# Optimization experiments

Hardware: AMD Instinct MI355X
Metric: run time of the kernel (lower is better)

## Reference

```python
import jax, jax.numpy as jnp
import numpy as np

B, T, D = 1, 4096, 1024
H, DK, DV, L = 16, 64, 64, 32
ROT_SCALE = 1.0  # rotary_pos_scale default


def _rotate_half(x):
    # '... (j d) -> ... j d' with j=2, then cat((-x2, x1))
    x1, x2 = jnp.split(x, 2, axis=-1)
    return jnp.concatenate((-x2, x1), axis=-1)


def _apply_rope(freqs, x, scale):
    # freqs: [T, L] broadcasts over leading dims of x [..., T, L]
    return x * jnp.cos(freqs) * scale + _rotate_half(x) * jnp.sin(freqs) * scale


def setup_inputs() -> dict:
    key = jax.random.key(0)
    ks = jax.random.split(key, 9)
    q = jax.random.normal(ks[0], (B, T, D), jnp.float32)
    k = jax.random.normal(ks[1], (B, T, D), jnp.float32)
    v = jax.random.normal(ks[2], (B, T, D), jnp.float32)
    mask = jnp.tril(jnp.ones((T, T), dtype=bool))  # causal [T, T]
    rotary_freqs = jax.random.normal(ks[3], (T, L), jnp.float32)
    s = 0.02
    w_q = jax.random.normal(ks[4], (H * DK, D), jnp.float32) * s
    w_k = jax.random.normal(ks[5], (H * DK, D), jnp.float32) * s
    w_v = jax.random.normal(ks[6], (H * DV, D), jnp.float32) * s
    w_o = jax.random.normal(ks[7], (D, H * DV), jnp.float32) * s
    return {"q": q, "k": k, "v": v, "mask": mask, "rotary_freqs": rotary_freqs,
            "w_q": w_q, "w_k": w_k, "w_v": w_v, "w_o": w_o}


def reference(q, k, v, mask, rotary_freqs, w_q, w_k, w_v, w_o):
    # project and split heads: '... T (H k) -> ... H T k'
    def heads(x, w, dh):
        y = jnp.einsum('btd,ed->bte', x, w)
        return y.reshape(B, T, H, dh).transpose(0, 2, 1, 3)  # [B,H,T,dh]

    q_i = heads(q, w_q, DK)
    k_i = heads(k, w_k, DK)
    v_i = heads(v, w_v, DV)

    # rotary pos emb on first L dims of q, k AND v (unusual: v too)
    q_scale, k_scale = ROT_SCALE, ROT_SCALE ** (-1.0)

    def rope(x, scale):
        xl, xr = x[..., :L], x[..., L:]
        return jnp.concatenate((_apply_rope(rotary_freqs, xl, scale), xr), axis=-1)

    q_i = rope(q_i, q_scale)
    k_i = rope(k_i, k_scale)
    v_i = rope(v_i, k_scale)

    s_qk = jnp.einsum('bhik,bhjk->bhij', q_i, k_i) / (DK ** 0.5)
    neg = -jnp.finfo(s_qk.dtype).max
    s_qk = jnp.where(mask, s_qk, neg)  # mask broadcasts [T,T] -> [B,H,T,T]
    attn = jax.nn.softmax(s_qk, axis=-1)
    vals = jnp.einsum('bhij,bhjv->bhiv', attn, v_i)
    vals = vals.transpose(0, 2, 1, 3).reshape(B, T, H * DV)  # '... H T v -> ... T (H v)'
    out = jnp.einsum('bte,oe->bto', vals, w_o)
    return out
```

## Files before the change

kernel.cpp:

```cpp
#include <hip/hip_runtime.h>

typedef unsigned short u16;
typedef unsigned int u32;
typedef short bf16x8 __attribute__((ext_vector_type(8)));
typedef float f32x4 __attribute__((ext_vector_type(4)));
typedef unsigned short u16x4 __attribute__((ext_vector_type(4)));
typedef unsigned short u16x8 __attribute__((ext_vector_type(8)));

__device__ __forceinline__ u16 f32_to_bf16(float f) {
    u32 u = __float_as_uint(f);
    u += 0x7FFFu + ((u >> 16) & 1u);
    return (u16)(u >> 16);
}
__device__ __forceinline__ short f32_to_bf16_trunc(float f) {
    return (short)(__float_as_uint(f) >> 16);
}

__device__ __forceinline__ void gl_lds16(const u16* g, u16* l) {
    __builtin_amdgcn_global_load_lds(
        (const __attribute__((address_space(1))) u32*)g,
        (__attribute__((address_space(3))) u32*)l, 16, 0, 0);
}

struct CastArgs {
    const float* src[7];
    u16* dst[7];
    int n4[7];
};

__global__ __launch_bounds__(256) void cast_kernel(CastArgs a) {
    const int y = blockIdx.y;
    const float* s = a.src[y];
    u16* d = a.dst[y];
    const int n4 = a.n4[y];
    for (int i = blockIdx.x * blockDim.x + threadIdx.x; i < n4; i += gridDim.x * blockDim.x) {
        f32x4 v = *(const f32x4*)&s[(size_t)i * 4];
        u16x4 o = { f32_to_bf16(v[0]), f32_to_bf16(v[1]), f32_to_bf16(v[2]), f32_to_bf16(v[3]) };
        *(u16x4*)&d[(size_t)i * 4] = o;
    }
}

#define GK 1024
#define GN 1024
#define GM 4096

__global__ __launch_bounds__(256) void gemm_rope(
    const u16* __restrict__ A0, const u16* __restrict__ A1, const u16* __restrict__ A2,
    const u16* __restrict__ W0, const u16* __restrict__ W1, const u16* __restrict__ W2,
    u16* __restrict__ C0, u16* __restrict__ C1, u16* __restrict__ C2,
    const float* __restrict__ freqs)
{
    __shared__ u16 SM[8192];
    u16* As = SM;
    u16* Bs = SM + 4096;

    const int z = blockIdx.z;
    const u16* A = (z == 0) ? A0 : ((z == 1) ? A1 : A2);
    const u16* W = (z == 0) ? W0 : ((z == 1) ? W1 : W2);
    u16* Cb      = (z == 0) ? C0 : ((z == 1) ? C1 : C2);
    const float ascale = (z == 0) ? 0.125f : 1.0f;

    const int tid  = threadIdx.x;
    const int w    = tid >> 6;
    const int lane = tid & 63;
    const int quad = lane >> 4;
    const int l16  = lane & 15;
    const int m0 = blockIdx.x * 128;
    const int n0 = blockIdx.y * 128;
    const int wm = (w >> 1) * 64;
    const int wn = (w & 1) * 64;

    const int sr = tid >> 2;
    const int sc = (tid & 3) * 8;
    const size_t aoff0 = (size_t)(m0 + sr) * GK + sc;
    const size_t aoff1 = aoff0 + (size_t)64 * GK;
    const size_t boff0 = (size_t)(n0 + sr) * GK + sc;
    const size_t boff1 = boff0 + (size_t)64 * GK;
    u16* ldsA0 = &As[w * 512];
    u16* ldsA1 = &As[2048 + w * 512];
    u16* ldsB0 = &Bs[w * 512];
    u16* ldsB1 = &Bs[2048 + w * 512];

    f32x4 acc[4][4];
    for (int i = 0; i < 4; i++)
        for (int j = 0; j < 4; j++) acc[i][j] = 0.f;

    for (int k0 = 0; k0 < GK; k0 += 32) {
        gl_lds16(A + aoff0 + k0, ldsA0);
        gl_lds16(A + aoff1 + k0, ldsA1);
        gl_lds16(W + boff0 + k0, ldsB0);
        gl_lds16(W + boff1 + k0, ldsB1);
        __syncthreads();

        bf16x8 af[4], bfr[4];
        for (int t = 0; t < 4; t++) {
            af[t]  = *(const bf16x8*)&As[(wm + t * 16 + l16) * 32 + quad * 8];
            bfr[t] = *(const bf16x8*)&Bs[(wn + t * 16 + l16) * 32 + quad * 8];
        }
        for (int mt = 0; mt < 4; mt++)
            for (int nt = 0; nt < 4; nt++)
                acc[mt][nt] = __builtin_amdgcn_mfma_f32_16x16x32_bf16(
                    af[mt], bfr[nt], acc[mt][nt], 0, 0, 0);
        __syncthreads();
    }
    u16* tr = SM + w * 1152;

    const int hh = (n0 + wn) >> 6;
    const size_t tb = (size_t)hh * 262144 + (size_t)((m0 + wm) >> 6) * 4096;

    if (z != 2) {
        for (int mt = 0; mt < 4; mt++) {
            #pragma unroll
            for (int r = 0; r < 4; r++) {
                int m = m0 + wm + mt * 16 + quad * 4 + r;
                float v0 = acc[mt][0][r];
                float v1 = acc[mt][1][r];
                float f0 = freqs[m * 32 + l16];
                float f1 = freqs[m * 32 + 16 + l16];
                float s0, c0, s1, c1;
                __sincosf(f0, &s0, &c0);
                __sincosf(f1, &s1, &c1);
                int row = quad * 4 + r;
                tr[row * 72 + l16]      = f32_to_bf16((v0 * c0 - v1 * s0) * ascale);
                tr[row * 72 + 16 + l16] = f32_to_bf16((v1 * c1 + v0 * s1) * ascale);
                tr[row * 72 + 32 + l16] = f32_to_bf16(acc[mt][2][r] * ascale);
                tr[row * 72 + 48 + l16] = f32_to_bf16(acc[mt][3][r] * ascale);
            }
            u16x8 va = *(const u16x8*)&tr[l16 * 72 + quad * 16];
            u16x8 vb = *(const u16x8*)&tr[l16 * 72 + quad * 16 + 8];
            if (z == 0) {
                size_t base = (size_t)(m0 + wm + mt * 16 + l16) * GN + n0 + wn + quad * 16;
                *(u16x8*)&Cb[base]     = va;
                *(u16x8*)&Cb[base + 8] = vb;
            } else {
                size_t base = tb + (size_t)(quad >> 1) * 2048
                            + (size_t)(mt * 16 + l16) * 32 + (quad & 1) * 16;
                *(u16x8*)&Cb[base]     = va;
                *(u16x8*)&Cb[base + 8] = vb;
            }
        }
    } else {
        for (int mt = 0; mt < 4; mt++) {
            float o0[4], o1[4];
            for (int r = 0; r < 4; r++) {
                int m = m0 + wm + mt * 16 + quad * 4 + r;
                float v0 = acc[mt][0][r];
                float v1 = acc[mt][1][r];
                float f0 = freqs[m * 32 + l16];
                float f1 = freqs[m * 32 + 16 + l16];
                float s0, c0, s1, c1;
                __sincosf(f0, &s0, &c0);
                __sincosf(f1, &s1, &c1);
                o0[r] = v0 * c0 - v1 * s0;
                o1[r] = v1 * c1 + v0 * s1;
            }
            const int ks = mt >> 1;
            const int sl = 4 * (mt & 1) + 8 * quad;
            const size_t hb = tb + (size_t)ks * 2048 + sl;
            u16x4 u;
            u = { f32_to_bf16(o0[0]), f32_to_bf16(o0[1]), f32_to_bf16(o0[2]), f32_to_bf16(o0[3]) };
            *(u16x4*)&Cb[hb + (size_t)l16 * 32] = u;
            u = { f32_to_bf16(o1[0]), f32_to_bf16(o1[1]), f32_to_bf16(o1[2]), f32_to_bf16(o1[3]) };
            *(u16x4*)&Cb[hb + (size_t)(16 + l16) * 32] = u;
            u = { f32_to_bf16(acc[mt][2][0]), f32_to_bf16(acc[mt][2][1]),
                  f32_to_bf16(acc[mt][2][2]), f32_to_bf16(acc[mt][2][3]) };
            *(u16x4*)&Cb[hb + (size_t)(32 + l16) * 32] = u;
            u = { f32_to_bf16(acc[mt][3][0]), f32_to_bf16(acc[mt][3][1]),
                  f32_to_bf16(acc[mt][3][2]), f32_to_bf16(acc[mt][3][3]) };
            *(u16x4*)&Cb[hb + (size_t)(48 + l16) * 32] = u;
        }
    }
}

__global__ __launch_bounds__(256) void gemm_out(
    const u16* __restrict__ A, const u16* __restrict__ W, float* __restrict__ C)
{
    __shared__ u16 SM[8704];
    u16* As = SM;
    u16* Bs = SM + 2048;

    const int tid  = threadIdx.x;
    const int w    = tid >> 6;
    const int lane = tid & 63;
    const int quad = lane >> 4;
    const int l16  = lane & 15;
    const int m0 = blockIdx.x * 64;
    const int n0 = blockIdx.y * 128;
    const int wm = (w >> 1) * 32;
    const int wn = (w & 1) * 64;

    const size_t aoff  = (size_t)(m0 + (tid >> 2)) * GK + (tid & 3) * 8;
    const size_t boff0 = (size_t)(n0 + (tid >> 2)) * GK + (tid & 3) * 8;
    const size_t boff1 = boff0 + (size_t)64 * GK;
    u16* ldsA  = &As[w * 512];
    u16* ldsB0 = &Bs[w * 512];
    u16* ldsB1 = &Bs[2048 + w * 512];

    f32x4 acc[2][4];
    for (int i = 0; i < 2; i++)
        for (int j = 0; j < 4; j++) acc[i][j] = 0.f;

    for (int k0 = 0; k0 < GK; k0 += 32) {
        gl_lds16(A + aoff + k0, ldsA);
        gl_lds16(W + boff0 + k0, ldsB0);
        gl_lds16(W + boff1 + k0, ldsB1);
        __syncthreads();

        bf16x8 af[2], bfr[4];
        for (int t = 0; t < 2; t++)
            af[t] = *(const bf16x8*)&As[(wm + t * 16 + l16) * 32 + quad * 8];
        for (int t = 0; t < 4; t++)
            bfr[t] = *(const bf16x8*)&Bs[(wn + t * 16 + l16) * 32 + quad * 8];
        for (int mt = 0; mt < 2; mt++)
            for (int nt = 0; nt < 4; nt++)
                acc[mt][nt] = __builtin_amdgcn_mfma_f32_16x16x32_bf16(
                    af[mt], bfr[nt], acc[mt][nt], 0, 0, 0);
        __syncthreads();
    }

    float* tr = (float*)SM + w * 1088;
    for (int mt = 0; mt < 2; mt++) {
        #pragma unroll
        for (int nt = 0; nt < 4; nt++)
            #pragma unroll
            for (int r = 0; r < 4; r++)
                tr[(quad * 4 + r) * 68 + nt * 16 + l16] = acc[mt][nt][r];
        size_t base = (size_t)(m0 + wm + mt * 16 + l16) * GN + n0 + wn + quad * 16;
        #pragma unroll
        for (int c = 0; c < 4; c++) {
            f32x4 v = *(const f32x4*)&tr[l16 * 68 + quad * 16 + c * 4];
            *(f32x4*)&C[base + c * 4] = v;
        }
    }
}

__global__ __launch_bounds__(256, 2) void attn_kernel(
    const u16* __restrict__ Qb, const u16* __restrict__ KT,
    const u16* __restrict__ VTg, u16* __restrict__ valsb)
{
    __shared__ u16 KV[2][8192];
    __shared__ float Ow[4][16 * 68];

    const int tid  = threadIdx.x;
    const int w    = tid >> 6;
    const int lane = tid & 63;
    const int quad = lane >> 4;
    const int l16  = lane & 15;
    const int HD = 1024;

    const int id  = blockIdx.x;
    const int h   = (id & 7) * 2 + ((id >> 3) & 1);
    const int idx = id >> 4;
    const int p   = (idx < 16) ? idx : (47 - idx);
    const int jt  = (w < 2) ? (63 - p) : p;
    const int kb_end = 63 - p;
    const int kb_me  = (w < 2) ? (63 - p) : p;
    const int qbase  = (w & 1) * 32;

    const u16* kt = KT  + (size_t)h * 262144;
    const u16* vt = VTg + (size_t)h * 262144;

    bf16x8 bq[2][2];
    #pragma unroll
    for (int qt = 0; qt < 2; qt++)
        #pragma unroll
        for (int ks = 0; ks < 2; ks++)
            bq[qt][ks] = *(const bf16x8*)&Qb[(size_t)(jt * 64 + qbase + qt * 16 + l16) * HD
                                             + h * 64 + ks * 32 + quad * 8];

    f32x4 o[2][4];
    #pragma unroll
    for (int qt = 0; qt < 2; qt++)
        #pragma unroll
        for (int nv = 0; nv < 4; nv++) o[qt][nv] = 0.f;
    float lsum[2] = { 0.f, 0.f };

    #pragma unroll
    for (int i = 0; i < 2; i++) {
        gl_lds16(kt + i * 2048 + w * 512 + lane * 8, &KV[0][i * 2048 + w * 512]);
        gl_lds16(vt + i * 2048 + w * 512 + lane * 8, &KV[0][4096 + i * 2048 + w * 512]);
    }

    for (int kb = 0; kb <= kb_end; kb++) {
        __syncthreads();
        if (kb < kb_end) {
            const int nb = (kb + 1) & 1;
            const u16* ksrc = kt + (size_t)(kb + 1) * 4096;
            const u16* vsrc = vt + (size_t)(kb + 1) * 4096;
            #pragma unroll
            for (int i = 0; i < 2; i++) {
                gl_lds16(ksrc + i * 2048 + w * 512 + lane * 8, &KV[nb][i * 2048 + w * 512]);
                gl_lds16(vsrc + i * 2048 + w * 512 + lane * 8, &KV[nb][4096 + i * 2048 + w * 512]);
            }
        }
        if (kb > kb_me) continue;

        const u16* Ksb = &KV[kb & 1][0];
        const u16* Vsb = &KV[kb & 1][4096];

        f32x4 s[2][4];
        #pragma unroll
        for (int nt = 0; nt < 4; nt++) {
            bf16x8 ak0 = *(const bf16x8*)&Ksb[(nt * 16 + l16) * 32 + quad * 8];
            bf16x8 ak1 = *(const bf16x8*)&Ksb[2048 + (nt * 16 + l16) * 32 + quad * 8];
            #pragma unroll
            for (int qt = 0; qt < 2; qt++) {
                f32x4 z4 = { 0.f, 0.f, 0.f, 0.f };
                s[qt][nt] = __builtin_amdgcn_mfma_f32_16x16x32_bf16(ak0, bq[qt][0], z4, 0, 0, 0);
                s[qt][nt] = __builtin_amdgcn_mfma_f32_16x16x32_bf16(ak1, bq[qt][1], s[qt][nt], 0, 0, 0);
            }
        }

        if (kb == kb_me) {
            #pragma unroll
            for (int qt = 0; qt < 2; qt++) {
                const int ql = qbase + qt * 16 + l16;
                #pragma unroll
                for (int nt = 0; nt < 4; nt++)
                    #pragma unroll
                    for (int r = 0; r < 4; r++)
                        if (nt * 16 + quad * 4 + r > ql) s[qt][nt][r] = -1e30f;
            }
        }

        bf16x8 av[8];
        #pragma unroll
        for (int nv = 0; nv < 4; nv++) {
            av[nv * 2]     = *(const bf16x8*)&Vsb[(nv * 16 + l16) * 32 + quad * 8];
            av[nv * 2 + 1] = *(const bf16x8*)&Vsb[2048 + (nv * 16 + l16) * 32 + quad * 8];
        }

        #pragma unroll
        for (int qt = 0; qt < 2; qt++) {
            float ls = 0.f;
            #pragma unroll
            for (int nt = 0; nt < 4; nt++)
                #pragma unroll
                for (int r = 0; r < 4; r++) {
                    float pe = __expf(s[qt][nt][r] - 16.f);
                    s[qt][nt][r] = pe;
                    ls += pe;
                }
            lsum[qt] += ls;

            bf16x8 bp0 = { f32_to_bf16_trunc(s[qt][0][0]), f32_to_bf16_trunc(s[qt][0][1]),
                           f32_to_bf16_trunc(s[qt][0][2]), f32_to_bf16_trunc(s[qt][0][3]),
                           f32_to_bf16_trunc(s[qt][1][0]), f32_to_bf16_trunc(s[qt][1][1]),
                           f32_to_bf16_trunc(s[qt][1][2]), f32_to_bf16_trunc(s[qt][1][3]) };
            bf16x8 bp1 = { f32_to_bf16_trunc(s[qt][2][0]), f32_to_bf16_trunc(s[qt][2][1]),
                           f32_to_bf16_trunc(s[qt][2][2]), f32_to_bf16_trunc(s[qt][2][3]),
                           f32_to_bf16_trunc(s[qt][3][0]), f32_to_bf16_trunc(s[qt][3][1]),
                           f32_to_bf16_trunc(s[qt][3][2]), f32_to_bf16_trunc(s[qt][3][3]) };
            #pragma unroll
            for (int nv = 0; nv < 4; nv++) {
                o[qt][nv] = __builtin_amdgcn_mfma_f32_16x16x32_bf16(av[nv * 2], bp0, o[qt][nv], 0, 0, 0);
                o[qt][nv] = __builtin_amdgcn_mfma_f32_16x16x32_bf16(av[nv * 2 + 1], bp1, o[qt][nv], 0, 0, 0);
            }
        }
    }

    float* myOw = Ow[w];
    #pragma unroll
    for (int qt = 0; qt < 2; qt++) {
        float ls = lsum[qt];
        ls += __shfl_xor(ls, 16);
        ls += __shfl_xor(ls, 32);
        const float linv = 1.f / ls;
        #pragma unroll
        for (int nv = 0; nv < 4; nv++)
            #pragma unroll
            for (int r = 0; r < 4; r++)
                myOw[l16 * 68 + nv * 16 + quad * 4 + r] = o[qt][nv][r] * linv;
        #pragma unroll
        for (int i = 0; i < 4; i++) {
            int row = i * 4 + quad;
            f32x4 vv = *(const f32x4*)&myOw[row * 68 + l16 * 4];
            u16x4 u = { f32_to_bf16(vv[0]), f32_to_bf16(vv[1]), f32_to_bf16(vv[2]), f32_to_bf16(vv[3]) };
            *(u16x4*)&valsb[(size_t)(jt * 64 + qbase + qt * 16 + row) * HD + h * 64 + l16 * 4] = u;
        }
    }
}

extern "C" void kernel_launch(void* const* d_in, const int* in_sizes, int n_in,
                              void* d_out, int out_size, void* d_ws, size_t ws_size,
                              hipStream_t stream) {
    const float* q     = (const float*)d_in[0];
    const float* k     = (const float*)d_in[1];
    const float* v     = (const float*)d_in[2];
    const float* freqs = (const float*)d_in[4];
    const float* wq    = (const float*)d_in[5];
    const float* wk    = (const float*)d_in[6];
    const float* wv    = (const float*)d_in[7];
    const float* wo    = (const float*)d_in[8];

    u16* B = (u16*)d_ws;
    u16* qc  = B;
    u16* kc  = B + (size_t)4194304;
    u16* vc  = B + (size_t)8388608;
    u16* wqc = B + (size_t)12582912;
    u16* wkc = B + (size_t)13631488;
    u16* wvc = B + (size_t)14680064;
    u16* woc = B + (size_t)15728640;
    u16* Qb  = B + (size_t)16777216;
    u16* KT  = B + (size_t)20971520;
    u16* VT  = B + (size_t)25165824;
    u16* valsb = qc;

    CastArgs ca;
    ca.src[0] = q;  ca.dst[0] = qc;  ca.n4[0] = 1048576;
    ca.src[1] = k;  ca.dst[1] = kc;  ca.n4[1] = 1048576;
    ca.src[2] = v;  ca.dst[2] = vc;  ca.n4[2] = 1048576;
    ca.src[3] = wq; ca.dst[3] = wqc; ca.n4[3] = 262144;
    ca.src[4] = wk; ca.dst[4] = wkc; ca.n4[4] = 262144;
    ca.src[5] = wv; ca.dst[5] = wvc; ca.n4[5] = 262144;
    ca.src[6] = wo; ca.dst[6] = woc; ca.n4[6] = 262144;
    cast_kernel<<<dim3(1024, 7), 256, 0, stream>>>(ca);

    gemm_rope<<<dim3(32, 8, 3), 256, 0, stream>>>(
        qc, kc, vc, wqc, wkc, wvc, Qb, KT, VT, freqs);

    attn_kernel<<<dim3(512), 256, 0, stream>>>(Qb, KT, VT, valsb);

    gemm_out<<<dim3(64, 8), 256, 0, stream>>>(valsb, woc, (float*)d_out);
}
```

Baseline: 289.0 us.

## Swizzle LDS tiles, precompute rope sincos, use exp2 softmax, rebalance causal attention blocks

```diff
diff --git a/kernel.cpp b/kernel.cpp
--- a/kernel.cpp
+++ b/kernel.cpp
@@ -4,6 +4,7 @@
 typedef unsigned int u32;
 typedef short bf16x8 __attribute__((ext_vector_type(8)));
 typedef float f32x4 __attribute__((ext_vector_type(4)));
+typedef float f32x2 __attribute__((ext_vector_type(2)));
 typedef unsigned short u16x4 __attribute__((ext_vector_type(4)));
 typedef unsigned short u16x8 __attribute__((ext_vector_type(8)));
 
@@ -15,6 +16,11 @@
 __device__ __forceinline__ short f32_to_bf16_trunc(float f) {
     return (short)(__float_as_uint(f) >> 16);
 }
+__device__ __forceinline__ float fast_exp2(float x) {
+    float r;
+    asm("v_exp_f32 %0, %1" : "=v"(r) : "v"(x));
+    return r;
+}
 
 __device__ __forceinline__ void gl_lds16(const u16* g, u16* l) {
     __builtin_amdgcn_global_load_lds(
@@ -22,17 +28,32 @@
         (__attribute__((address_space(3))) u32*)l, 16, 0, 0);
 }
 
+
 struct CastArgs {
-    const float* src[7];
-    u16* dst[7];
-    int n4[7];
+    const float* src[8];
+    u16* dst[8];
+    int n4[8];
 };
 
 __global__ __launch_bounds__(256) void cast_kernel(CastArgs a) {
     const int y = blockIdx.y;
     const float* s = a.src[y];
+    const int n4 = a.n4[y];
+    if (y == 7) {
+        f32x2* out = (f32x2*)a.dst[7];
+        for (int i = blockIdx.x * blockDim.x + threadIdx.x; i < n4; i += gridDim.x * blockDim.x) {
+            f32x4 f = *(const f32x4*)&s[(size_t)i * 4];
+            #pragma unroll
+            for (int j = 0; j < 4; j++) {
+                float sn, cs;
+                __sincosf(f[j], &sn, &cs);
+                f32x2 v = { cs, sn };
+                out[(size_t)i * 4 + j] = v;
+            }
+        }
+        return;
+    }
     u16* d = a.dst[y];
-    const int n4 = a.n4[y];
     for (int i = blockIdx.x * blockDim.x + threadIdx.x; i < n4; i += gridDim.x * blockDim.x) {
         f32x4 v = *(const f32x4*)&s[(size_t)i * 4];
         u16x4 o = { f32_to_bf16(v[0]), f32_to_bf16(v[1]), f32_to_bf16(v[2]), f32_to_bf16(v[3]) };
@@ -48,7 +69,7 @@
     const u16* __restrict__ A0, const u16* __restrict__ A1, const u16* __restrict__ A2,
     const u16* __restrict__ W0, const u16* __restrict__ W1, const u16* __restrict__ W2,
     u16* __restrict__ C0, u16* __restrict__ C1, u16* __restrict__ C2,
-    const float* __restrict__ freqs)
+    const f32x2* __restrict__ csn)
 {
     __shared__ u16 SM[8192];
     u16* As = SM;
@@ -58,7 +79,7 @@
     const u16* A = (z == 0) ? A0 : ((z == 1) ? A1 : A2);
     const u16* W = (z == 0) ? W0 : ((z == 1) ? W1 : W2);
     u16* Cb      = (z == 0) ? C0 : ((z == 1) ? C1 : C2);
-    const float ascale = (z == 0) ? 0.125f : 1.0f;
+    const float ascale = (z == 0) ? 0.18033688011f : 1.0f;
 
     const int tid  = threadIdx.x;
     const int w    = tid >> 6;
@@ -71,7 +92,7 @@
     const int wn = (w & 1) * 64;
 
     const int sr = tid >> 2;
-    const int sc = (tid & 3) * 8;
+    const int sc = (((tid & 3) ^ ((tid >> 3) & 3))) * 8;
     const size_t aoff0 = (size_t)(m0 + sr) * GK + sc;
     const size_t aoff1 = aoff0 + (size_t)64 * GK;
     const size_t boff0 = (size_t)(n0 + sr) * GK + sc;
@@ -81,6 +102,8 @@
     u16* ldsB0 = &Bs[w * 512];
     u16* ldsB1 = &Bs[2048 + w * 512];
 
+    const int csw = (quad ^ ((l16 >> 1) & 3)) * 8;
+
     f32x4 acc[4][4];
     for (int i = 0; i < 4; i++)
         for (int j = 0; j < 4; j++) acc[i][j] = 0.f;
@@ -94,8 +117,8 @@
 
         bf16x8 af[4], bfr[4];
         for (int t = 0; t < 4; t++) {
-            af[t]  = *(const bf16x8*)&As[(wm + t * 16 + l16) * 32 + quad * 8];
-            bfr[t] = *(const bf16x8*)&Bs[(wn + t * 16 + l16) * 32 + quad * 8];
+            af[t]  = *(const bf16x8*)&As[(wm + t * 16 + l16) * 32 + csw];
+            bfr[t] = *(const bf16x8*)&Bs[(wn + t * 16 + l16) * 32 + csw];
         }
         for (int mt = 0; mt < 4; mt++)
             for (int nt = 0; nt < 4; nt++)
@@ -115,14 +138,11 @@
                 int m = m0 + wm + mt * 16 + quad * 4 + r;
                 float v0 = acc[mt][0][r];
                 float v1 = acc[mt][1][r];
-                float f0 = freqs[m * 32 + l16];
-                float f1 = freqs[m * 32 + 16 + l16];
-                float s0, c0, s1, c1;
-                __sincosf(f0, &s0, &c0);
-                __sincosf(f1, &s1, &c1);
+                f32x2 c0 = csn[m * 32 + l16];
+                f32x2 c1 = csn[m * 32 + 16 + l16];
                 int row = quad * 4 + r;
-                tr[row * 72 + l16]      = f32_to_bf16((v0 * c0 - v1 * s0) * ascale);
-                tr[row * 72 + 16 + l16] = f32_to_bf16((v1 * c1 + v0 * s1) * ascale);
+                tr[row * 72 + l16]      = f32_to_bf16((v0 * c0[0] - v1 * c0[1]) * ascale);
+                tr[row * 72 + 16 + l16] = f32_to_bf16((v1 * c1[0] + v0 * c1[1]) * ascale);
                 tr[row * 72 + 32 + l16] = f32_to_bf16(acc[mt][2][r] * ascale);
                 tr[row * 72 + 48 + l16] = f32_to_bf16(acc[mt][3][r] * ascale);
             }
@@ -146,13 +166,10 @@
                 int m = m0 + wm + mt * 16 + quad * 4 + r;
                 float v0 = acc[mt][0][r];
                 float v1 = acc[mt][1][r];
-                float f0 = freqs[m * 32 + l16];
-                float f1 = freqs[m * 32 + 16 + l16];
-                float s0, c0, s1, c1;
-                __sincosf(f0, &s0, &c0);
-                __sincosf(f1, &s1, &c1);
-                o0[r] = v0 * c0 - v1 * s0;
-                o1[r] = v1 * c1 + v0 * s1;
+                f32x2 c0 = csn[m * 32 + l16];
+                f32x2 c1 = csn[m * 32 + 16 + l16];
+                o0[r] = v0 * c0[0] - v1 * c0[1];
+                o1[r] = v1 * c1[0] + v0 * c1[1];
             }
             const int ks = mt >> 1;
             const int sl = 4 * (mt & 1) + 8 * quad;
@@ -189,12 +206,16 @@
     const int wm = (w >> 1) * 32;
     const int wn = (w & 1) * 64;
 
-    const size_t aoff  = (size_t)(m0 + (tid >> 2)) * GK + (tid & 3) * 8;
-    const size_t boff0 = (size_t)(n0 + (tid >> 2)) * GK + (tid & 3) * 8;
+    const int sr = tid >> 2;
+    const int sc = (((tid & 3) ^ ((tid >> 3) & 3))) * 8;
+    const size_t aoff  = (size_t)(m0 + sr) * GK + sc;
+    const size_t boff0 = (size_t)(n0 + sr) * GK + sc;
     const size_t boff1 = boff0 + (size_t)64 * GK;
     u16* ldsA  = &As[w * 512];
     u16* ldsB0 = &Bs[w * 512];
     u16* ldsB1 = &Bs[2048 + w * 512];
+
+    const int csw = (quad ^ ((l16 >> 1) & 3)) * 8;
 
     f32x4 acc[2][4];
     for (int i = 0; i < 2; i++)
@@ -208,9 +229,9 @@
 
         bf16x8 af[2], bfr[4];
         for (int t = 0; t < 2; t++)
-            af[t] = *(const bf16x8*)&As[(wm + t * 16 + l16) * 32 + quad * 8];
+            af[t] = *(const bf16x8*)&As[(wm + t * 16 + l16) * 32 + csw];
         for (int t = 0; t < 4; t++)
-            bfr[t] = *(const bf16x8*)&Bs[(wn + t * 16 + l16) * 32 + quad * 8];
+            bfr[t] = *(const bf16x8*)&Bs[(wn + t * 16 + l16) * 32 + csw];
         for (int mt = 0; mt < 2; mt++)
             for (int nt = 0; nt < 4; nt++)
                 acc[mt][nt] = __builtin_amdgcn_mfma_f32_16x16x32_bf16(
@@ -251,21 +272,23 @@
     const int id  = blockIdx.x;
     const int h   = (id & 7) * 2 + ((id >> 3) & 1);
     const int idx = id >> 4;
-    const int p   = (idx < 16) ? idx : (47 - idx);
-    const int jt  = (w < 2) ? (63 - p) : p;
-    const int kb_end = 63 - p;
-    const int kb_me  = (w < 2) ? (63 - p) : p;
-    const int qbase  = (w & 1) * 32;
+    const int g   = (idx < 16) ? idx : (47 - idx);
 
     const u16* kt = KT  + (size_t)h * 262144;
     const u16* vt = VTg + (size_t)h * 262144;
+
+    const int kb_end = 2 * g + 1;
+    const int jt     = 2 * g + (w >> 1);
+    const int qb32   = (w & 1) * 32;
+    const int dmaoff = (lane >> 2) * 32 + ((lane & 3) ^ ((lane >> 3) & 3)) * 8;
+    const int csw    = (quad ^ ((l16 >> 1) & 3)) * 8;
 
     bf16x8 bq[2][2];
     #pragma unroll
     for (int qt = 0; qt < 2; qt++)
         #pragma unroll
         for (int ks = 0; ks < 2; ks++)
-            bq[qt][ks] = *(const bf16x8*)&Qb[(size_t)(jt * 64 + qbase + qt * 16 + l16) * HD
+            bq[qt][ks] = *(const bf16x8*)&Qb[(size_t)(jt * 64 + qb32 + qt * 16 + l16) * HD
                                              + h * 64 + ks * 32 + quad * 8];
 
     f32x4 o[2][4];
@@ -277,8 +300,8 @@
 
     #pragma unroll
     for (int i = 0; i < 2; i++) {
-        gl_lds16(kt + i * 2048 + w * 512 + lane * 8, &KV[0][i * 2048 + w * 512]);
-        gl_lds16(vt + i * 2048 + w * 512 + lane * 8, &KV[0][4096 + i * 2048 + w * 512]);
+        gl_lds16(kt + i * 2048 + w * 512 + dmaoff, &KV[0][i * 2048 + w * 512]);
+        gl_lds16(vt + i * 2048 + w * 512 + dmaoff, &KV[0][4096 + i * 2048 + w * 512]);
     }
 
     for (int kb = 0; kb <= kb_end; kb++) {
@@ -289,32 +312,32 @@
             const u16* vsrc = vt + (size_t)(kb + 1) * 4096;
             #pragma unroll
             for (int i = 0; i < 2; i++) {
-                gl_lds16(ksrc + i * 2048 + w * 512 + lane * 8, &KV[nb][i * 2048 + w * 512]);
-                gl_lds16(vsrc + i * 2048 + w * 512 + lane * 8, &KV[nb][4096 + i * 2048 + w * 512]);
-            }
-        }
-        if (kb > kb_me) continue;
+                gl_lds16(ksrc + i * 2048 + w * 512 + dmaoff, &KV[nb][i * 2048 + w * 512]);
+                gl_lds16(vsrc + i * 2048 + w * 512 + dmaoff, &KV[nb][4096 + i * 2048 + w * 512]);
+            }
+        }
+        if (kb > jt) continue;
 
         const u16* Ksb = &KV[kb & 1][0];
         const u16* Vsb = &KV[kb & 1][4096];
 
+        const f32x4 minit = { -16.f, -16.f, -16.f, -16.f };
         f32x4 s[2][4];
         #pragma unroll
         for (int nt = 0; nt < 4; nt++) {
-            bf16x8 ak0 = *(const bf16x8*)&Ksb[(nt * 16 + l16) * 32 + quad * 8];
-            bf16x8 ak1 = *(const bf16x8*)&Ksb[2048 + (nt * 16 + l16) * 32 + quad * 8];
+            bf16x8 ak0 = *(const bf16x8*)&Ksb[(nt * 16 + l16) * 32 + csw];
+            bf16x8 ak1 = *(const bf16x8*)&Ksb[2048 + (nt * 16 + l16) * 32 + csw];
             #pragma unroll
             for (int qt = 0; qt < 2; qt++) {
-                f32x4 z4 = { 0.f, 0.f, 0.f, 0.f };
-                s[qt][nt] = __builtin_amdgcn_mfma_f32_16x16x32_bf16(ak0, bq[qt][0], z4, 0, 0, 0);
+                s[qt][nt] = __builtin_amdgcn_mfma_f32_16x16x32_bf16(ak0, bq[qt][0], minit, 0, 0, 0);
                 s[qt][nt] = __builtin_amdgcn_mfma_f32_16x16x32_bf16(ak1, bq[qt][1], s[qt][nt], 0, 0, 0);
             }
         }
 
-        if (kb == kb_me) {
+        if (kb == jt) {
             #pragma unroll
             for (int qt = 0; qt < 2; qt++) {
-                const int ql = qbase + qt * 16 + l16;
+                const int ql = qb32 + qt * 16 + l16;
                 #pragma unroll
                 for (int nt = 0; nt < 4; nt++)
                     #pragma unroll
@@ -326,8 +349,8 @@
         bf16x8 av[8];
         #pragma unroll
         for (int nv = 0; nv < 4; nv++) {
-            av[nv * 2]     = *(const bf16x8*)&Vsb[(nv * 16 + l16) * 32 + quad * 8];
-            av[nv * 2 + 1] = *(const bf16x8*)&Vsb[2048 + (nv * 16 + l16) * 32 + quad * 8];
+            av[nv * 2]     = *(const bf16x8*)&Vsb[(nv * 16 + l16) * 32 + csw];
+            av[nv * 2 + 1] = *(const bf16x8*)&Vsb[2048 + (nv * 16 + l16) * 32 + csw];
         }
 
         #pragma unroll
@@ -337,7 +360,7 @@
             for (int nt = 0; nt < 4; nt++)
                 #pragma unroll
                 for (int r = 0; r < 4; r++) {
-                    float pe = __expf(s[qt][nt][r] - 16.f);
+                    float pe = fast_exp2(s[qt][nt][r]);
                     s[qt][nt][r] = pe;
                     ls += pe;
                 }
@@ -376,7 +399,7 @@
             int row = i * 4 + quad;
             f32x4 vv = *(const f32x4*)&myOw[row * 68 + l16 * 4];
             u16x4 u = { f32_to_bf16(vv[0]), f32_to_bf16(vv[1]), f32_to_bf16(vv[2]), f32_to_bf16(vv[3]) };
-            *(u16x4*)&valsb[(size_t)(jt * 64 + qbase + qt * 16 + row) * HD + h * 64 + l16 * 4] = u;
+            *(u16x4*)&valsb[(size_t)(jt * 64 + qb32 + qt * 16 + row) * HD + h * 64 + l16 * 4] = u;
         }
     }
 }
@@ -404,20 +427,22 @@
     u16* Qb  = B + (size_t)16777216;
     u16* KT  = B + (size_t)20971520;
     u16* VT  = B + (size_t)25165824;
+    f32x2* CSN = (f32x2*)(B + (size_t)29360128);
     u16* valsb = qc;
 
     CastArgs ca;
-    ca.src[0] = q;  ca.dst[0] = qc;  ca.n4[0] = 1048576;
-    ca.src[1] = k;  ca.dst[1] = kc;  ca.n4[1] = 1048576;
-    ca.src[2] = v;  ca.dst[2] = vc;  ca.n4[2] = 1048576;
-    ca.src[3] = wq; ca.dst[3] = wqc; ca.n4[3] = 262144;
-    ca.src[4] = wk; ca.dst[4] = wkc; ca.n4[4] = 262144;
-    ca.src[5] = wv; ca.dst[5] = wvc; ca.n4[5] = 262144;
-    ca.src[6] = wo; ca.dst[6] = woc; ca.n4[6] = 262144;
-    cast_kernel<<<dim3(1024, 7), 256, 0, stream>>>(ca);
+    ca.src[0] = q;     ca.dst[0] = qc;        ca.n4[0] = 1048576;
+    ca.src[1] = k;     ca.dst[1] = kc;        ca.n4[1] = 1048576;
+    ca.src[2] = v;     ca.dst[2] = vc;        ca.n4[2] = 1048576;
+    ca.src[3] = wq;    ca.dst[3] = wqc;       ca.n4[3] = 262144;
+    ca.src[4] = wk;    ca.dst[4] = wkc;       ca.n4[4] = 262144;
+    ca.src[5] = wv;    ca.dst[5] = wvc;       ca.n4[5] = 262144;
+    ca.src[6] = wo;    ca.dst[6] = woc;       ca.n4[6] = 262144;
+    ca.src[7] = freqs; ca.dst[7] = (u16*)CSN; ca.n4[7] = 32768;
+    cast_kernel<<<dim3(1024, 8), 256, 0, stream>>>(ca);
 
     gemm_rope<<<dim3(32, 8, 3), 256, 0, stream>>>(
-        qc, kc, vc, wqc, wkc, wvc, Qb, KT, VT, freqs);
+        qc, kc, vc, wqc, wkc, wvc, Qb, KT, VT, CSN);
 
     attn_kernel<<<dim3(512), 256, 0, stream>>>(Qb, KT, VT, valsb);
 
```

Result: faster. 281.2 us (-2.7%).
